# Kernel tuning notes

Measured on AMD Instinct MI355X. Metric: run time of the kernel, lower is better.

The kernel has to match this reference:

```python
import jax, jax.numpy as jnp
import numpy as np


def _ln(x):
    m = jnp.mean(x, axis=-1, keepdims=True)
    v = jnp.var(x, axis=-1, keepdims=True)
    return (x - m) * jax.lax.rsqrt(v + 1e-5)


def _forward(ql, cl, plm, ada_g_w, ada_g_b, ada_b_w, wq, bq, wk, wv, z_ln_g, z_ln_b, wz, wg, wo, sg_w, sg_b, ada2_g_w, ada2_g_b, ada2_b_w, ff1, ff2, ff3, sg2_w, sg2_b, n_queries, n_keys):
    B, N, C = ql.shape
    NB, _, D = wq.shape
    H = wz.shape[-1]
    DH = D // H
    # AF3-style 32x128 blocked local attention bias (additive mask), as in source
    centers = jnp.arange(N // n_queries + 1, dtype=jnp.float32) * n_queries + (n_queries / 2 - 0.5)
    pos = jnp.arange(N, dtype=jnp.float32)
    row = jnp.abs(pos[:, None] - centers[None, :]) < n_queries / 2   # [N, n_centers]
    col = jnp.abs(pos[:, None] - centers[None, :]) < n_keys / 2     # [N, n_centers]
    BIG = jnp.float32(1e10)
    blm = jnp.sum((row[:, None, :] & col[None, :, :]).astype(jnp.float32), axis=-1) * BIG - BIG  # [N, N], 0 or -1e10
    s_ln = _ln(cl)  # conditioning signal, shared LN across blocks
    a = ql
    for i in range(NB):  # DiffusionTransformer (AF3 Alg 23)
        # AttentionPairBias with AdaLN conditioning (Alg 24/26)
        x = jax.nn.sigmoid(s_ln @ ada_g_w[i] + ada_g_b[i]) * _ln(a) + s_ln @ ada_b_w[i]
        q = (x @ wq[i] + bq[i]).reshape(B, N, H, DH)
        k = (x @ wk[i]).reshape(B, N, H, DH)
        v = (x @ wv[i]).reshape(B, N, H, DH)
        zb = jnp.einsum('bqkc,ch->bhqk', _ln(plm) * z_ln_g[i] + z_ln_b[i], wz[i])  # pair bias
        logits = jnp.einsum('bqhd,bkhd->bhqk', q, k) * (1.0 / np.sqrt(DH)) + zb + blm[None, None]
        p = jax.nn.softmax(logits, axis=-1)
        o = jnp.einsum('bhqk,bkhd->bqhd', p, v)
        g = jax.nn.sigmoid(x @ wg[i]).reshape(B, N, H, DH)
        attn = (g * o).reshape(B, N, D) @ wo[i]
        b_out = jax.nn.sigmoid(s_ln @ sg_w[i] + sg_b[i]) * attn  # adaLN-zero style output gate
        # ConditionedTransitionBlock (Alg 25, SwiGLU)
        y = jax.nn.sigmoid(s_ln @ ada2_g_w[i] + ada2_g_b[i]) * _ln(a) + s_ln @ ada2_b_w[i]
        ff = jax.nn.silu(y @ ff1[i]) * (y @ ff2[i])
        t = jax.nn.sigmoid(s_ln @ sg2_w[i] + sg2_b[i]) * (ff @ ff3[i])
        a = b_out + t
    return a


def setup_inputs() -> dict:
    key = jax.random.key(0)
    B, N, C, CZ = 1, 3072, 128, 16
    H, DH, NB, CT = 4, 32, 3, 256  # CT = n_transition * C
    D = H * DH
    ks = jax.random.split(key, 32)
    it = iter(range(32))
    def r(shape, s=0.02):
        return jax.random.normal(ks[next(it)], shape, dtype=jnp.float32) * s
    inp = {
        'ql': jax.random.normal(ks[next(it)], (B, N, C), jnp.float32),
        'cl': jax.random.normal(ks[next(it)], (B, N, C), jnp.float32),
        'plm': jax.random.normal(ks[next(it)], (B, N, N, CZ), jnp.float32),
        'ada_g_w': r((NB, C, C)), 'ada_g_b': jnp.zeros((NB, C), jnp.float32), 'ada_b_w': r((NB, C, C)),
        'wq': r((NB, C, D)), 'bq': jnp.zeros((NB, D), jnp.float32), 'wk': r((NB, C, D)), 'wv': r((NB, C, D)),
        'z_ln_g': jnp.ones((NB, CZ), jnp.float32), 'z_ln_b': jnp.zeros((NB, CZ), jnp.float32), 'wz': r((NB, CZ, H)),
        'wg': r((NB, C, D)), 'wo': r((NB, D, C)),
        'sg_w': r((NB, C, C)), 'sg_b': jnp.full((NB, C), -2.0, jnp.float32),
        'ada2_g_w': r((NB, C, C)), 'ada2_g_b': jnp.zeros((NB, C), jnp.float32), 'ada2_b_w': r((NB, C, C)),
        'ff1': r((NB, C, CT)), 'ff2': r((NB, C, CT)), 'ff3': r((NB, CT, C)),
        'sg2_w': r((NB, C, C)), 'sg2_b': jnp.full((NB, C), -2.0, jnp.float32),
        'n_queries': 32, 'n_keys': 128,
    }
    return inp


def reference(ql, cl, plm, ada_g_w, ada_g_b, ada_b_w, wq, bq, wk, wv, z_ln_g, z_ln_b, wz, wg, wo, sg_w, sg_b, ada2_g_w, ada2_g_b, ada2_b_w, ff1, ff2, ff3, sg2_w, sg2_b, n_queries, n_keys):
    return _forward(ql, cl, plm, ada_g_w, ada_g_b, ada_b_w, wq, bq, wk, wv, z_ln_g, z_ln_b, wz, wg, wo, sg_w, sg_b, ada2_g_w, ada2_g_b, ada2_b_w, ff1, ff2, ff3, sg2_w, sg2_b, n_queries, n_keys)
```

## Files before the change

### kernel.cpp

```cpp
#include <hip/hip_runtime.h>
#include <cmath>

#define NTOK 3072
#define NBLK 3
#define PSS 133

__device__ __forceinline__ float sig(float v) { return 1.0f / (1.0f + expf(-v)); }

struct Params {
    const float *ql, *cl, *plm;
    const float *ada_g_w, *ada_g_b, *ada_b_w;
    const float *wq, *bq, *wk, *wv;
    const float *z_ln_g, *z_ln_b, *wz;
    const float *wg, *wo, *sg_w, *sg_b;
    const float *ada2_g_w, *ada2_g_b, *ada2_b_w;
    const float *ff1, *ff2, *ff3, *sg2_w, *sg2_b;
    float *qkvg, *ffb, *zb, *G, *bout4, *tpart;
    float *out;
};

__device__ __forceinline__ float4 ln_row32(float4 v)
{
    float s = v.x + v.y + v.z + v.w;
#pragma unroll
    for (int m = 1; m < 32; m <<= 1) s += __shfl_xor(s, m);
    float mean = s * (1.0f / 128.0f);
    float d0 = v.x - mean, d1 = v.y - mean, d2 = v.z - mean, d3 = v.w - mean;
    float var = d0 * d0 + d1 * d1 + d2 * d2 + d3 * d3;
#pragma unroll
    for (int m = 1; m < 32; m <<= 1) var += __shfl_xor(var, m);
    float rs = 1.0f / sqrtf(var * (1.0f / 128.0f) + 1e-5f);
    return make_float4(d0 * rs, d1 * rs, d2 * rs, d3 * rs);
}

__global__ __launch_bounds__(256) void k0_cond(Params P)
{
    int tid = threadIdx.x, bid = blockIdx.x;
    const size_t NC = (size_t)NTOK * 128;
    if (bid < 1728) {
        __shared__ __align__(16) float smA[32 * 132];
        int x8 = bid & 7, rest = bid >> 3;
        int tl = rest % 12, unit = rest / 12;
        int kind = unit % 6, i = unit / 6;
        int row0 = (x8 * 12 + tl) * 32;
#pragma unroll
        for (int it = 0; it < 4; it++) {
            int fo = (tid + it * 256) * 4, r = fo >> 7, c = fo & 127;
            *(float4*)&smA[r * 132 + c] = *(const float4*)&P.cl[(size_t)(row0 + r) * 128 + c];
        }
        __syncthreads();
        int hw = tid >> 5, cq = (tid & 31) * 4;
#pragma unroll
        for (int rr = 0; rr < 4; rr++) {
            int r = hw * 4 + rr;
            float4 n = ln_row32(*(float4*)&smA[r * 132 + cq]);
            *(float4*)&smA[r * 132 + cq] = n;
        }
        __syncthreads();
        const float* W; const float* bias = nullptr; bool dosig = false;
        switch (kind) {
            case 0:  W = P.ada_g_w  + (size_t)i * 16384; bias = P.ada_g_b  + i * 128; dosig = true; break;
            case 1:  W = P.ada_b_w  + (size_t)i * 16384; break;
            case 2:  W = P.ada2_g_w + (size_t)i * 16384; bias = P.ada2_g_b + i * 128; dosig = true; break;
            case 3:  W = P.ada2_b_w + (size_t)i * 16384; break;
            case 4:  W = P.sg_w     + (size_t)i * 16384; bias = P.sg_b     + i * 128; dosig = true; break;
            default: W = P.sg2_w    + (size_t)i * 16384; bias = P.sg2_b    + i * 128; dosig = true; break;
        }
        W += cq;
        float acc[4][4] = {};
#pragma unroll 8
        for (int k = 0; k < 128; k++) {
            float4 w4 = *(const float4*)(W + (size_t)k * 128);
#pragma unroll
            for (int rr = 0; rr < 4; rr++) {
                float a = smA[(hw * 4 + rr) * 132 + k];
                acc[rr][0] = fmaf(a, w4.x, acc[rr][0]);
                acc[rr][1] = fmaf(a, w4.y, acc[rr][1]);
                acc[rr][2] = fmaf(a, w4.z, acc[rr][2]);
                acc[rr][3] = fmaf(a, w4.w, acc[rr][3]);
            }
        }
        float4 b4 = bias ? *(const float4*)&bias[cq] : make_float4(0, 0, 0, 0);
        float* dst = P.G + (size_t)(kind * NBLK + i) * NC;
#pragma unroll
        for (int rr = 0; rr < 4; rr++) {
            float4 o = make_float4(acc[rr][0] + b4.x, acc[rr][1] + b4.y,
                                   acc[rr][2] + b4.z, acc[rr][3] + b4.w);
            if (dosig) { o.x = sig(o.x); o.y = sig(o.y); o.z = sig(o.z); o.w = sig(o.w); }
            *(float4*)&dst[(size_t)(row0 + hw * 4 + rr) * 128 + cq] = o;
        }
    } else {
        __shared__ __align__(16) float wzg[204];
        int b2 = bid - 1728;
        int x8 = b2 & 7, rest = b2 >> 3;
        int jl = rest >> 2, kkc = rest & 3;
        int j = x8 * 12 + jl;
        if (tid < 192) {
            int i3 = tid >> 6, rem = tid & 63, c = rem >> 2, h = rem & 3;
            wzg[(i3 * 16 + c) * 4 + h] = P.z_ln_g[i3 * 16 + c] * P.wz[(i3 * 16 + c) * 4 + h];
        }
        if (tid < 12) {
            int i3 = tid >> 2, h = tid & 3;
            float s = 0.0f;
            for (int c = 0; c < 16; c++) s += P.z_ln_b[i3 * 16 + c] * P.wz[(i3 * 16 + c) * 4 + h];
            wzg[192 + tid] = s;
        }
        __syncthreads();
        int kstart = max(0, j * 32 - 48);
        int W = min(NTOK, j * 32 + 80) - kstart;
#pragma unroll
        for (int it = 0; it < 4; it++) {
            int idx = tid + it * 256;
            int qi = idx >> 5, kk = kkc * 32 + (idx & 31);
            if (kk >= W) continue;
            int q = j * 32 + qi;
            const float* src = P.plm + ((size_t)q * NTOK + (size_t)(kstart + kk)) * 16;
            float xv[16];
            *(float4*)(xv + 0)  = *(const float4*)(src + 0);
            *(float4*)(xv + 4)  = *(const float4*)(src + 4);
            *(float4*)(xv + 8)  = *(const float4*)(src + 8);
            *(float4*)(xv + 12) = *(const float4*)(src + 12);
            float s = 0.0f;
#pragma unroll
            for (int c = 0; c < 16; c++) s += xv[c];
            float mean = s * (1.0f / 16.0f);
            float var = 0.0f;
#pragma unroll
            for (int c = 0; c < 16; c++) { float d = xv[c] - mean; var += d * d; }
            float rs = 1.0f / sqrtf(var * (1.0f / 16.0f) + 1e-5f);
#pragma unroll
            for (int c = 0; c < 16; c++) xv[c] = (xv[c] - mean) * rs;
#pragma unroll
            for (int i3 = 0; i3 < NBLK; i3++) {
#pragma unroll
                for (int h = 0; h < 4; h++) {
                    float o = wzg[192 + i3 * 4 + h];
#pragma unroll
                    for (int c = 0; c < 16; c++) o = fmaf(xv[c], wzg[(i3 * 16 + c) * 4 + h], o);
                    P.zb[((size_t)(i3 * 4 + h) * NTOK + q) * 128 + kk] = o;
                }
            }
        }
    }
}

__global__ __launch_bounds__(256) void kA_pre(Params P, int i)
{
    __shared__ __align__(16) float smX[32 * 132];
    const size_t NC = (size_t)NTOK * 128;
    int tid = threadIdx.x, bid = blockIdx.x;
    int x8 = bid & 7, rest = bid >> 3;
    int tl = rest % 12, u = rest / 12;
    int row0 = (x8 * 12 + tl) * 32;
    int hw = tid >> 5, cq = (tid & 31) * 4;
    const float* Gg = P.G + (size_t)(((u < 4 ? 0 : 2) * NBLK) + i) * NC;
    const float* Gb = P.G + (size_t)(((u < 4 ? 1 : 3) * NBLK) + i) * NC;
    const float* G4p = P.G + (size_t)(4 * NBLK + (i - 1)) * NC;
#pragma unroll
    for (int rr = 0; rr < 4; rr++) {
        int r = row0 + hw * 4 + rr;
        float4 a4;
        if (i == 0) {
            a4 = *(const float4*)&P.ql[(size_t)r * 128 + cq];
        } else {
            size_t off = (size_t)r * 128 + cq;
            float4 p0 = *(const float4*)&P.bout4[off];
            float4 p1 = *(const float4*)&P.bout4[NC + off];
            float4 p2 = *(const float4*)&P.bout4[2 * NC + off];
            float4 p3 = *(const float4*)&P.bout4[3 * NC + off];
            float4 tp = *(const float4*)&P.tpart[off];
            float4 gs = *(const float4*)&G4p[off];
            a4.x = fmaf(gs.x, p0.x + p1.x + p2.x + p3.x, tp.x);
            a4.y = fmaf(gs.y, p0.y + p1.y + p2.y + p3.y, tp.y);
            a4.z = fmaf(gs.z, p0.z + p1.z + p2.z + p3.z, tp.z);
            a4.w = fmaf(gs.w, p0.w + p1.w + p2.w + p3.w, tp.w);
        }
        float4 ln4 = ln_row32(a4);
        float4 g4 = *(const float4*)&Gg[(size_t)r * 128 + cq];
        float4 b4 = *(const float4*)&Gb[(size_t)r * 128 + cq];
        float4 x4;
        x4.x = fmaf(g4.x, ln4.x, b4.x);
        x4.y = fmaf(g4.y, ln4.y, b4.y);
        x4.z = fmaf(g4.z, ln4.z, b4.z);
        x4.w = fmaf(g4.w, ln4.w, b4.w);
        *(float4*)&smX[(hw * 4 + rr) * 132 + cq] = x4;
    }
    __syncthreads();
    if (u < 4) {
        const float* W = (u == 0 ? P.wq : u == 1 ? P.wk : u == 2 ? P.wv : P.wg)
                         + (size_t)i * 16384 + cq;
        float acc[4][4] = {};
#pragma unroll 8
        for (int k = 0; k < 128; k++) {
            float4 w4 = *(const float4*)(W + (size_t)k * 128);
#pragma unroll
            for (int rr = 0; rr < 4; rr++) {
                float a = smX[(hw * 4 + rr) * 132 + k];
                acc[rr][0] = fmaf(a, w4.x, acc[rr][0]);
                acc[rr][1] = fmaf(a, w4.y, acc[rr][1]);
                acc[rr][2] = fmaf(a, w4.z, acc[rr][2]);
                acc[rr][3] = fmaf(a, w4.w, acc[rr][3]);
            }
        }
        float4 b4 = (u == 0) ? *(const float4*)&P.bq[(size_t)i * 128 + cq]
                             : make_float4(0, 0, 0, 0);
#pragma unroll
        for (int rr = 0; rr < 4; rr++) {
            int r = row0 + hw * 4 + rr;
            *(float4*)&P.qkvg[(size_t)r * 512 + u * 128 + cq] =
                make_float4(acc[rr][0] + b4.x, acc[rr][1] + b4.y,
                            acc[rr][2] + b4.z, acc[rr][3] + b4.w);
        }
    } else {
        int ch = (u - 4) * 128;
        const float* W1 = P.ff1 + (size_t)i * 32768 + ch + cq;
        const float* W2 = P.ff2 + (size_t)i * 32768 + ch + cq;
        float a1[4][4] = {}, a2[4][4] = {};
#pragma unroll 4
        for (int k = 0; k < 128; k++) {
            float4 w14 = *(const float4*)(W1 + (size_t)k * 256);
            float4 w24 = *(const float4*)(W2 + (size_t)k * 256);
#pragma unroll
            for (int rr = 0; rr < 4; rr++) {
                float a = smX[(hw * 4 + rr) * 132 + k];
                a1[rr][0] = fmaf(a, w14.x, a1[rr][0]);
                a1[rr][1] = fmaf(a, w14.y, a1[rr][1]);
                a1[rr][2] = fmaf(a, w14.z, a1[rr][2]);
                a1[rr][3] = fmaf(a, w14.w, a1[rr][3]);
                a2[rr][0] = fmaf(a, w24.x, a2[rr][0]);
                a2[rr][1] = fmaf(a, w24.y, a2[rr][1]);
                a2[rr][2] = fmaf(a, w24.z, a2[rr][2]);
                a2[rr][3] = fmaf(a, w24.w, a2[rr][3]);
            }
        }
#pragma unroll
        for (int rr = 0; rr < 4; rr++) {
            int r = row0 + hw * 4 + rr;
            float4 o;
            o.x = a1[rr][0] * sig(a1[rr][0]) * a2[rr][0];
            o.y = a1[rr][1] * sig(a1[rr][1]) * a2[rr][1];
            o.z = a1[rr][2] * sig(a1[rr][2]) * a2[rr][2];
            o.w = a1[rr][3] * sig(a1[rr][3]) * a2[rr][3];
            *(float4*)&P.ffb[(size_t)r * 256 + ch + cq] = o;
        }
    }
}

__global__ __launch_bounds__(256) void kB_attn(Params P, int i)
{
    __shared__ __align__(16) float sm[11344];
    const size_t NC = (size_t)NTOK * 128;
    int tid = threadIdx.x, bid = blockIdx.x;
    if (bid < 768) {
        float* ks = sm;
        float* vs = sm + 4608;
        float* ps = sm + 9216;
        int x8 = bid & 7, g = bid >> 3;
        int jl = g >> 3, rem = g & 7;
        int h = rem >> 1, qh = rem & 1;
        int jglob = x8 * 12 + jl;
        int q0 = jglob * 32 + qh * 16;
        int kstart = max(0, jglob * 32 - 48);
        int W = min(NTOK, jglob * 32 + 80) - kstart;
        for (int idx = tid; idx < W * 8; idx += 256) {
            int kk = idx >> 3, d = (idx & 7) * 4;
            const float* base = &P.qkvg[(size_t)(kstart + kk) * 512 + 128 + h * 32 + d];
            float4 tK = *(const float4*)base;
            float4 tV = *(const float4*)(base + 128);
            *(float4*)&ks[kk * 36 + d] = tK;
            *(float4*)&vs[kk * 36 + d] = tV;
        }
        const float* zbase = &P.zb[((size_t)(i * 4 + h) * NTOK + q0) * 128];
#pragma unroll
        for (int it = 0; it < 2; it++) {
            int idx = tid + it * 256;
            int r = idx >> 5, c4 = (idx & 31) * 4;
            float4 z4 = *(const float4*)&zbase[(size_t)r * 128 + c4];
            ps[r * PSS + c4]     = z4.x;
            ps[r * PSS + c4 + 1] = z4.y;
            ps[r * PSS + c4 + 2] = z4.z;
            ps[r * PSS + c4 + 3] = z4.w;
        }
        int qi = tid & 15, kg = tid >> 4;
        float qreg[32];
        {
            const float* qp = &P.qkvg[(size_t)(q0 + qi) * 512 + h * 32];
#pragma unroll
            for (int d4 = 0; d4 < 8; d4++) {
                float4 tq = *(const float4*)(qp + d4 * 4);
                qreg[d4 * 4] = tq.x; qreg[d4 * 4 + 1] = tq.y;
                qreg[d4 * 4 + 2] = tq.z; qreg[d4 * 4 + 3] = tq.w;
            }
        }
        __syncthreads();
        const float scale = 0.17677669529663687f;
#pragma unroll
        for (int t2 = 0; t2 < 8; t2++) {
            int kk = kg + t2 * 16;
            if (kk < W) {
                float acc = 0.0f;
#pragma unroll
                for (int d4 = 0; d4 < 8; d4++) {
                    float4 kv = *(const float4*)&ks[kk * 36 + d4 * 4];
                    acc = fmaf(qreg[d4 * 4 + 0], kv.x, acc);
                    acc = fmaf(qreg[d4 * 4 + 1], kv.y, acc);
                    acc = fmaf(qreg[d4 * 4 + 2], kv.z, acc);
                    acc = fmaf(qreg[d4 * 4 + 3], kv.w, acc);
                }
                ps[qi * PSS + kk] = fmaf(acc, scale, ps[qi * PSS + kk]);
            }
        }
        __syncthreads();
        {
            int row = tid >> 4, sub = tid & 15;
            float m = -3.0e38f;
            for (int kk = sub; kk < W; kk += 16) m = fmaxf(m, ps[row * PSS + kk]);
#pragma unroll
            for (int s2 = 1; s2 < 16; s2 <<= 1) m = fmaxf(m, __shfl_xor(m, s2));
            float ssum = 0.0f;
            for (int kk = sub; kk < W; kk += 16) {
                float e = expf(ps[row * PSS + kk] - m);
                ps[row * PSS + kk] = e; ssum += e;
            }
#pragma unroll
            for (int s2 = 1; s2 < 16; s2 <<= 1) ssum += __shfl_xor(ssum, s2);
            float rinv = 1.0f / ssum;
            for (int kk = sub; kk < W; kk += 16) ps[row * PSS + kk] *= rinv;
        }
        __syncthreads();
        {
            int dg = tid >> 4, d0 = dg * 2;
            float o0 = 0.0f, o1 = 0.0f, o0b = 0.0f, o1b = 0.0f;
            for (int kk = 0; kk + 1 < W; kk += 2) {
                float p0 = ps[qi * PSS + kk], p1 = ps[qi * PSS + kk + 1];
                float2 va = *(const float2*)&vs[kk * 36 + d0];
                float2 vb = *(const float2*)&vs[(kk + 1) * 36 + d0];
                o0  = fmaf(p0, va.x, o0);  o1  = fmaf(p0, va.y, o1);
                o0b = fmaf(p1, vb.x, o0b); o1b = fmaf(p1, vb.y, o1b);
            }
            if (W & 1) {
                float p0 = ps[qi * PSS + W - 1];
                float2 va = *(const float2*)&vs[(W - 1) * 36 + d0];
                o0 = fmaf(p0, va.x, o0); o1 = fmaf(p0, va.y, o1);
            }
            o0 += o0b; o1 += o1b;
            float2 g2 = *(const float2*)&P.qkvg[(size_t)(q0 + qi) * 512 + 384 + h * 32 + d0];
            ks[qi * 33 + d0]     = o0 * sig(g2.x);
            ks[qi * 33 + d0 + 1] = o1 * sig(g2.y);
        }
        __syncthreads();
        {
            int r = tid >> 4, ci = tid & 15;
            int c0 = ci * 8;
            const float* o_s = ks;
            const float* wop = P.wo + (size_t)i * 16384 + (size_t)(h * 32) * 128 + c0;
            float acc[8] = {};
#pragma unroll 4
            for (int d = 0; d < 32; d++) {
                float a = o_s[r * 33 + d];
                float4 w0 = *(const float4*)(wop + (size_t)d * 128);
                float4 w1 = *(const float4*)(wop + (size_t)d * 128 + 4);
                acc[0] = fmaf(a, w0.x, acc[0]); acc[1] = fmaf(a, w0.y, acc[1]);
                acc[2] = fmaf(a, w0.z, acc[2]); acc[3] = fmaf(a, w0.w, acc[3]);
                acc[4] = fmaf(a, w1.x, acc[4]); acc[5] = fmaf(a, w1.y, acc[5]);
                acc[6] = fmaf(a, w1.z, acc[6]); acc[7] = fmaf(a, w1.w, acc[7]);
            }
            float* dst = P.bout4 + (size_t)h * NC + (size_t)(q0 + r) * 128 + c0;
            *(float4*)dst       = make_float4(acc[0], acc[1], acc[2], acc[3]);
            *(float4*)(dst + 4) = make_float4(acc[4], acc[5], acc[6], acc[7]);
        }
    } else {
        float* smC = sm;
        int b2 = bid - 768;
        int x8 = b2 & 7, rest = b2 >> 3;
        int tl = rest >> 1, chalf = rest & 1;
        int row0 = x8 * 384 + tl * 16;
#pragma unroll
        for (int it = 0; it < 4; it++) {
            int fo = (tid + it * 256) * 4, r = fo >> 8, c = fo & 255;
            *(float4*)&smC[r * 260 + c] = *(const float4*)&P.ffb[(size_t)(row0 + r) * 256 + c];
        }
        __syncthreads();
        int r = tid >> 4, c = chalf * 64 + (tid & 15) * 4;
        const float* f3_p = P.ff3 + (size_t)i * 32768 + c;
        float acc[4] = {};
#pragma unroll 8
        for (int k = 0; k < 256; k++) {
            float4 w4 = *(const float4*)(f3_p + (size_t)k * 128);
            float a = smC[r * 260 + k];
            acc[0] = fmaf(a, w4.x, acc[0]);
            acc[1] = fmaf(a, w4.y, acc[1]);
            acc[2] = fmaf(a, w4.z, acc[2]);
            acc[3] = fmaf(a, w4.w, acc[3]);
        }
        int row = row0 + r;
        float4 g5 = *(const float4*)&P.G[(size_t)(5 * NBLK + i) * NC + (size_t)row * 128 + c];
        *(float4*)&P.tpart[(size_t)row * 128 + c] =
            make_float4(g5.x * acc[0], g5.y * acc[1], g5.z * acc[2], g5.w * acc[3]);
    }
}

__global__ __launch_bounds__(256) void kC_out(Params P)
{
    const size_t NC = (size_t)NTOK * 128;
    int idx = blockIdx.x * 256 + threadIdx.x;
    int r = idx >> 5, cq = (idx & 31) * 4;
    size_t off = (size_t)r * 128 + cq;
    float4 p0 = *(const float4*)&P.bout4[off];
    float4 p1 = *(const float4*)&P.bout4[NC + off];
    float4 p2 = *(const float4*)&P.bout4[2 * NC + off];
    float4 p3 = *(const float4*)&P.bout4[3 * NC + off];
    float4 tp = *(const float4*)&P.tpart[off];
    float4 gs = *(const float4*)&P.G[(size_t)(4 * NBLK + (NBLK - 1)) * NC + off];
    float4 o;
    o.x = fmaf(gs.x, p0.x + p1.x + p2.x + p3.x, tp.x);
    o.y = fmaf(gs.y, p0.y + p1.y + p2.y + p3.y, tp.y);
    o.z = fmaf(gs.z, p0.z + p1.z + p2.z + p3.z, tp.z);
    o.w = fmaf(gs.w, p0.w + p1.w + p2.w + p3.w, tp.w);
    *(float4*)&P.out[off] = o;
}

extern "C" void kernel_launch(void* const* d_in, const int* in_sizes, int n_in,
                              void* d_out, int out_size, void* d_ws, size_t ws_size,
                              hipStream_t stream)
{
    Params P;
    P.ql       = (const float*)d_in[0];
    P.cl       = (const float*)d_in[1];
    P.plm      = (const float*)d_in[2];
    P.ada_g_w  = (const float*)d_in[3];
    P.ada_g_b  = (const float*)d_in[4];
    P.ada_b_w  = (const float*)d_in[5];
    P.wq       = (const float*)d_in[6];
    P.bq       = (const float*)d_in[7];
    P.wk       = (const float*)d_in[8];
    P.wv       = (const float*)d_in[9];
    P.z_ln_g   = (const float*)d_in[10];
    P.z_ln_b   = (const float*)d_in[11];
    P.wz       = (const float*)d_in[12];
    P.wg       = (const float*)d_in[13];
    P.wo       = (const float*)d_in[14];
    P.sg_w     = (const float*)d_in[15];
    P.sg_b     = (const float*)d_in[16];
    P.ada2_g_w = (const float*)d_in[17];
    P.ada2_g_b = (const float*)d_in[18];
    P.ada2_b_w = (const float*)d_in[19];
    P.ff1      = (const float*)d_in[20];
    P.ff2      = (const float*)d_in[21];
    P.ff3      = (const float*)d_in[22];
    P.sg2_w    = (const float*)d_in[23];
    P.sg2_b    = (const float*)d_in[24];

    float* ws = (float*)d_ws;
    const size_t NC = (size_t)NTOK * 128;
    P.qkvg  = ws;
    P.ffb   = ws + 4 * NC;
    P.zb    = ws + 6 * NC;
    P.G     = ws + 18 * NC;
    P.bout4 = ws + 36 * NC;
    P.tpart = ws + 40 * NC;
    P.out   = (float*)d_out;

    k0_cond<<<2112, 256, 0, stream>>>(P);
    for (int i = 0; i < NBLK; i++) {
        kA_pre<<<576, 256, 0, stream>>>(P, i);
        kB_attn<<<1152, 256, 0, stream>>>(P, i);
    }
    kC_out<<<384, 256, 0, stream>>>(P);
}
```

Baseline: 264.1 us.

## Fold deferred conditioning and pair-bias work into first pre-attention launch

The standalone conditioning kernel is reduced to computing only the block-0 AdaLN gate and shift projections. The other conditioning projections and the pair-bias computation move into the first kA_pre launch as extra thread blocks, so they run alongside block-0's QKV and FFN work. The u index is reversed so the FFN units are scheduled first. This shortens the serial prologue and fills the GPU better, at the cost of a larger, heterogeneous first launch with more shared memory per block.

```diff
diff --git a/kernel.cpp b/kernel.cpp
--- a/kernel.cpp
+++ b/kernel.cpp
@@ -33,66 +33,182 @@
     return make_float4(d0 * rs, d1 * rs, d2 * rs, d3 * rs);
 }
 
-__global__ __launch_bounds__(256) void k0_cond(Params P)
-{
+__device__ __forceinline__ void cond_unit(const Params& P, float* smA, int tid,
+                                          int kind, int i, int row0)
+{
+    const size_t NC = (size_t)NTOK * 128;
+#pragma unroll
+    for (int it = 0; it < 4; it++) {
+        int fo = (tid + it * 256) * 4, r = fo >> 7, c = fo & 127;
+        *(float4*)&smA[r * 132 + c] = *(const float4*)&P.cl[(size_t)(row0 + r) * 128 + c];
+    }
+    __syncthreads();
+    int hw = tid >> 5, cq = (tid & 31) * 4;
+#pragma unroll
+    for (int rr = 0; rr < 4; rr++) {
+        int r = hw * 4 + rr;
+        float4 n = ln_row32(*(float4*)&smA[r * 132 + cq]);
+        *(float4*)&smA[r * 132 + cq] = n;
+    }
+    __syncthreads();
+    const float* W; const float* bias = nullptr; bool dosig = false;
+    switch (kind) {
+        case 0:  W = P.ada_g_w  + (size_t)i * 16384; bias = P.ada_g_b  + i * 128; dosig = true; break;
+        case 1:  W = P.ada_b_w  + (size_t)i * 16384; break;
+        case 2:  W = P.ada2_g_w + (size_t)i * 16384; bias = P.ada2_g_b + i * 128; dosig = true; break;
+        case 3:  W = P.ada2_b_w + (size_t)i * 16384; break;
+        case 4:  W = P.sg_w     + (size_t)i * 16384; bias = P.sg_b     + i * 128; dosig = true; break;
+        default: W = P.sg2_w    + (size_t)i * 16384; bias = P.sg2_b    + i * 128; dosig = true; break;
+    }
+    W += cq;
+    float acc[4][4] = {};
+#pragma unroll 8
+    for (int k = 0; k < 128; k++) {
+        float4 w4 = *(const float4*)(W + (size_t)k * 128);
+#pragma unroll
+        for (int rr = 0; rr < 4; rr++) {
+            float a = smA[(hw * 4 + rr) * 132 + k];
+            acc[rr][0] = fmaf(a, w4.x, acc[rr][0]);
+            acc[rr][1] = fmaf(a, w4.y, acc[rr][1]);
+            acc[rr][2] = fmaf(a, w4.z, acc[rr][2]);
+            acc[rr][3] = fmaf(a, w4.w, acc[rr][3]);
+        }
+    }
+    float4 b4 = bias ? *(const float4*)&bias[cq] : make_float4(0, 0, 0, 0);
+    float* dst = P.G + (size_t)(kind * NBLK + i) * NC;
+#pragma unroll
+    for (int rr = 0; rr < 4; rr++) {
+        float4 o = make_float4(acc[rr][0] + b4.x, acc[rr][1] + b4.y,
+                               acc[rr][2] + b4.z, acc[rr][3] + b4.w);
+        if (dosig) { o.x = sig(o.x); o.y = sig(o.y); o.z = sig(o.z); o.w = sig(o.w); }
+        *(float4*)&dst[(size_t)(row0 + hw * 4 + rr) * 128 + cq] = o;
+    }
+}
+
+__global__ __launch_bounds__(256) void kInit(Params P)
+{
+    __shared__ __align__(16) float smA[32 * 132];
     int tid = threadIdx.x, bid = blockIdx.x;
+    int x8 = bid & 7, rest = bid >> 3;
+    int tl = rest % 12, kind = rest / 12;
+    int row0 = (x8 * 12 + tl) * 32;
+    cond_unit(P, smA, tid, kind, 0, row0);
+}
+
+__global__ __launch_bounds__(256) void kA_pre(Params P, int i)
+{
+    __shared__ __align__(16) float smX[32 * 132];
+    __shared__ __align__(16) float wzg[204];
     const size_t NC = (size_t)NTOK * 128;
-    if (bid < 1728) {
-        __shared__ __align__(16) float smA[32 * 132];
+    int tid = threadIdx.x, bid = blockIdx.x;
+    if (bid < 576) {
         int x8 = bid & 7, rest = bid >> 3;
+        int tl = rest % 12, u = 5 - rest / 12;
+        int row0 = (x8 * 12 + tl) * 32;
+        int hw = tid >> 5, cq = (tid & 31) * 4;
+        const float* Gg = P.G + (size_t)(((u < 4 ? 0 : 2) * NBLK) + i) * NC;
+        const float* Gb = P.G + (size_t)(((u < 4 ? 1 : 3) * NBLK) + i) * NC;
+        const float* G4p = P.G + (size_t)(4 * NBLK + (i > 0 ? i - 1 : 0)) * NC;
+#pragma unroll
+        for (int rr = 0; rr < 4; rr++) {
+            int r = row0 + hw * 4 + rr;
+            size_t off = (size_t)r * 128 + cq;
+            float4 a4;
+            if (i == 0) {
+                a4 = *(const float4*)&P.ql[off];
+            } else {
+                float4 p0 = *(const float4*)&P.bout4[off];
+                float4 p1 = *(const float4*)&P.bout4[NC + off];
+                float4 p2 = *(const float4*)&P.bout4[2 * NC + off];
+                float4 p3 = *(const float4*)&P.bout4[3 * NC + off];
+                float4 tp = *(const float4*)&P.tpart[off];
+                float4 gs = *(const float4*)&G4p[off];
+                a4.x = fmaf(gs.x, p0.x + p1.x + p2.x + p3.x, tp.x);
+                a4.y = fmaf(gs.y, p0.y + p1.y + p2.y + p3.y, tp.y);
+                a4.z = fmaf(gs.z, p0.z + p1.z + p2.z + p3.z, tp.z);
+                a4.w = fmaf(gs.w, p0.w + p1.w + p2.w + p3.w, tp.w);
+            }
+            float4 ln4 = ln_row32(a4);
+            float4 g4 = *(const float4*)&Gg[off];
+            float4 b4 = *(const float4*)&Gb[off];
+            float4 x4;
+            x4.x = fmaf(g4.x, ln4.x, b4.x);
+            x4.y = fmaf(g4.y, ln4.y, b4.y);
+            x4.z = fmaf(g4.z, ln4.z, b4.z);
+            x4.w = fmaf(g4.w, ln4.w, b4.w);
+            *(float4*)&smX[(hw * 4 + rr) * 132 + cq] = x4;
+        }
+        __syncthreads();
+        if (u < 4) {
+            const float* W = (u == 0 ? P.wq : u == 1 ? P.wk : u == 2 ? P.wv : P.wg)
+                             + (size_t)i * 16384 + cq;
+            float acc[4][4] = {};
+#pragma unroll 8
+            for (int k = 0; k < 128; k++) {
+                float4 w4 = *(const float4*)(W + (size_t)k * 128);
+#pragma unroll
+                for (int rr = 0; rr < 4; rr++) {
+                    float a = smX[(hw * 4 + rr) * 132 + k];
+                    acc[rr][0] = fmaf(a, w4.x, acc[rr][0]);
+                    acc[rr][1] = fmaf(a, w4.y, acc[rr][1]);
+                    acc[rr][2] = fmaf(a, w4.z, acc[rr][2]);
+                    acc[rr][3] = fmaf(a, w4.w, acc[rr][3]);
+                }
+            }
+            float4 b4 = (u == 0) ? *(const float4*)&P.bq[(size_t)i * 128 + cq]
+                                 : make_float4(0, 0, 0, 0);
+#pragma unroll
+            for (int rr = 0; rr < 4; rr++) {
+                int r = row0 + hw * 4 + rr;
+                *(float4*)&P.qkvg[(size_t)r * 512 + u * 128 + cq] =
+                    make_float4(acc[rr][0] + b4.x, acc[rr][1] + b4.y,
+                                acc[rr][2] + b4.z, acc[rr][3] + b4.w);
+            }
+        } else {
+            int ch = (u - 4) * 128;
+            const float* W1 = P.ff1 + (size_t)i * 32768 + ch + cq;
+            const float* W2 = P.ff2 + (size_t)i * 32768 + ch + cq;
+            float a1[4][4] = {}, a2[4][4] = {};
+#pragma unroll 4
+            for (int k = 0; k < 128; k++) {
+                float4 w14 = *(const float4*)(W1 + (size_t)k * 256);
+                float4 w24 = *(const float4*)(W2 + (size_t)k * 256);
+#pragma unroll
+                for (int rr = 0; rr < 4; rr++) {
+                    float a = smX[(hw * 4 + rr) * 132 + k];
+                    a1[rr][0] = fmaf(a, w14.x, a1[rr][0]);
+                    a1[rr][1] = fmaf(a, w14.y, a1[rr][1]);
+                    a1[rr][2] = fmaf(a, w14.z, a1[rr][2]);
+                    a1[rr][3] = fmaf(a, w14.w, a1[rr][3]);
+                    a2[rr][0] = fmaf(a, w24.x, a2[rr][0]);
+                    a2[rr][1] = fmaf(a, w24.y, a2[rr][1]);
+                    a2[rr][2] = fmaf(a, w24.z, a2[rr][2]);
+                    a2[rr][3] = fmaf(a, w24.w, a2[rr][3]);
+                }
+            }
+#pragma unroll
+            for (int rr = 0; rr < 4; rr++) {
+                int r = row0 + hw * 4 + rr;
+                float4 o;
+                o.x = a1[rr][0] * sig(a1[rr][0]) * a2[rr][0];
+                o.y = a1[rr][1] * sig(a1[rr][1]) * a2[rr][1];
+                o.z = a1[rr][2] * sig(a1[rr][2]) * a2[rr][2];
+                o.w = a1[rr][3] * sig(a1[rr][3]) * a2[rr][3];
+                *(float4*)&P.ffb[(size_t)r * 256 + ch + cq] = o;
+            }
+        }
+    } else if (bid < 1920) {
+        int b2 = bid - 576;
+        int x8 = b2 & 7, rest = b2 >> 3;
         int tl = rest % 12, unit = rest / 12;
-        int kind = unit % 6, i = unit / 6;
+        int kind, il;
+        if (unit < 8) { kind = unit >> 1; il = 1 + (unit & 1); }
+        else          { int v = unit - 8; kind = 4 + v / 3; il = v % 3; }
         int row0 = (x8 * 12 + tl) * 32;
-#pragma unroll
-        for (int it = 0; it < 4; it++) {
-            int fo = (tid + it * 256) * 4, r = fo >> 7, c = fo & 127;
-            *(float4*)&smA[r * 132 + c] = *(const float4*)&P.cl[(size_t)(row0 + r) * 128 + c];
-        }
-        __syncthreads();
-        int hw = tid >> 5, cq = (tid & 31) * 4;
-#pragma unroll
-        for (int rr = 0; rr < 4; rr++) {
-            int r = hw * 4 + rr;
-            float4 n = ln_row32(*(float4*)&smA[r * 132 + cq]);
-            *(float4*)&smA[r * 132 + cq] = n;
-        }
-        __syncthreads();
-        const float* W; const float* bias = nullptr; bool dosig = false;
-        switch (kind) {
-            case 0:  W = P.ada_g_w  + (size_t)i * 16384; bias = P.ada_g_b  + i * 128; dosig = true; break;
-            case 1:  W = P.ada_b_w  + (size_t)i * 16384; break;
-            case 2:  W = P.ada2_g_w + (size_t)i * 16384; bias = P.ada2_g_b + i * 128; dosig = true; break;
-            case 3:  W = P.ada2_b_w + (size_t)i * 16384; break;
-            case 4:  W = P.sg_w     + (size_t)i * 16384; bias = P.sg_b     + i * 128; dosig = true; break;
-            default: W = P.sg2_w    + (size_t)i * 16384; bias = P.sg2_b    + i * 128; dosig = true; break;
-        }
-        W += cq;
-        float acc[4][4] = {};
-#pragma unroll 8
-        for (int k = 0; k < 128; k++) {
-            float4 w4 = *(const float4*)(W + (size_t)k * 128);
-#pragma unroll
-            for (int rr = 0; rr < 4; rr++) {
-                float a = smA[(hw * 4 + rr) * 132 + k];
-                acc[rr][0] = fmaf(a, w4.x, acc[rr][0]);
-                acc[rr][1] = fmaf(a, w4.y, acc[rr][1]);
-                acc[rr][2] = fmaf(a, w4.z, acc[rr][2]);
-                acc[rr][3] = fmaf(a, w4.w, acc[rr][3]);
-            }
-        }
-        float4 b4 = bias ? *(const float4*)&bias[cq] : make_float4(0, 0, 0, 0);
-        float* dst = P.G + (size_t)(kind * NBLK + i) * NC;
-#pragma unroll
-        for (int rr = 0; rr < 4; rr++) {
-            float4 o = make_float4(acc[rr][0] + b4.x, acc[rr][1] + b4.y,
-                                   acc[rr][2] + b4.z, acc[rr][3] + b4.w);
-            if (dosig) { o.x = sig(o.x); o.y = sig(o.y); o.z = sig(o.z); o.w = sig(o.w); }
-            *(float4*)&dst[(size_t)(row0 + hw * 4 + rr) * 128 + cq] = o;
-        }
+        cond_unit(P, smX, tid, kind, il, row0);
     } else {
-        __shared__ __align__(16) float wzg[204];
-        int b2 = bid - 1728;
-        int x8 = b2 & 7, rest = b2 >> 3;
+        int b3 = bid - 1920;
+        int x8 = b3 & 7, rest = b3 >> 3;
         int jl = rest >> 2, kkc = rest & 3;
         int j = x8 * 12 + jl;
         if (tid < 192) {
@@ -140,108 +256,6 @@
                     P.zb[((size_t)(i3 * 4 + h) * NTOK + q) * 128 + kk] = o;
                 }
             }
-        }
-    }
-}
-
-__global__ __launch_bounds__(256) void kA_pre(Params P, int i)
-{
-    __shared__ __align__(16) float smX[32 * 132];
-    const size_t NC = (size_t)NTOK * 128;
-    int tid = threadIdx.x, bid = blockIdx.x;
-    int x8 = bid & 7, rest = bid >> 3;
-    int tl = rest % 12, u = rest / 12;
-    int row0 = (x8 * 12 + tl) * 32;
-    int hw = tid >> 5, cq = (tid & 31) * 4;
-    const float* Gg = P.G + (size_t)(((u < 4 ? 0 : 2) * NBLK) + i) * NC;
-    const float* Gb = P.G + (size_t)(((u < 4 ? 1 : 3) * NBLK) + i) * NC;
-    const float* G4p = P.G + (size_t)(4 * NBLK + (i - 1)) * NC;
-#pragma unroll
-    for (int rr = 0; rr < 4; rr++) {
-        int r = row0 + hw * 4 + rr;
-        float4 a4;
-        if (i == 0) {
-            a4 = *(const float4*)&P.ql[(size_t)r * 128 + cq];
-        } else {
-            size_t off = (size_t)r * 128 + cq;
-            float4 p0 = *(const float4*)&P.bout4[off];
-            float4 p1 = *(const float4*)&P.bout4[NC + off];
-            float4 p2 = *(const float4*)&P.bout4[2 * NC + off];
-            float4 p3 = *(const float4*)&P.bout4[3 * NC + off];
-            float4 tp = *(const float4*)&P.tpart[off];
-            float4 gs = *(const float4*)&G4p[off];
-            a4.x = fmaf(gs.x, p0.x + p1.x + p2.x + p3.x, tp.x);
-            a4.y = fmaf(gs.y, p0.y + p1.y + p2.y + p3.y, tp.y);
-            a4.z = fmaf(gs.z, p0.z + p1.z + p2.z + p3.z, tp.z);
-            a4.w = fmaf(gs.w, p0.w + p1.w + p2.w + p3.w, tp.w);
-        }
-        float4 ln4 = ln_row32(a4);
-        float4 g4 = *(const float4*)&Gg[(size_t)r * 128 + cq];
-        float4 b4 = *(const float4*)&Gb[(size_t)r * 128 + cq];
-        float4 x4;
-        x4.x = fmaf(g4.x, ln4.x, b4.x);
-        x4.y = fmaf(g4.y, ln4.y, b4.y);
-        x4.z = fmaf(g4.z, ln4.z, b4.z);
-        x4.w = fmaf(g4.w, ln4.w, b4.w);
-        *(float4*)&smX[(hw * 4 + rr) * 132 + cq] = x4;
-    }
-    __syncthreads();
-    if (u < 4) {
-        const float* W = (u == 0 ? P.wq : u == 1 ? P.wk : u == 2 ? P.wv : P.wg)
-                         + (size_t)i * 16384 + cq;
-        float acc[4][4] = {};
-#pragma unroll 8
-        for (int k = 0; k < 128; k++) {
-            float4 w4 = *(const float4*)(W + (size_t)k * 128);
-#pragma unroll
-            for (int rr = 0; rr < 4; rr++) {
-                float a = smX[(hw * 4 + rr) * 132 + k];
-                acc[rr][0] = fmaf(a, w4.x, acc[rr][0]);
-                acc[rr][1] = fmaf(a, w4.y, acc[rr][1]);
-                acc[rr][2] = fmaf(a, w4.z, acc[rr][2]);
-                acc[rr][3] = fmaf(a, w4.w, acc[rr][3]);
-            }
-        }
-        float4 b4 = (u == 0) ? *(const float4*)&P.bq[(size_t)i * 128 + cq]
-                             : make_float4(0, 0, 0, 0);
-#pragma unroll
-        for (int rr = 0; rr < 4; rr++) {
-            int r = row0 + hw * 4 + rr;
-            *(float4*)&P.qkvg[(size_t)r * 512 + u * 128 + cq] =
-                make_float4(acc[rr][0] + b4.x, acc[rr][1] + b4.y,
-                            acc[rr][2] + b4.z, acc[rr][3] + b4.w);
-        }
-    } else {
-        int ch = (u - 4) * 128;
-        const float* W1 = P.ff1 + (size_t)i * 32768 + ch + cq;
-        const float* W2 = P.ff2 + (size_t)i * 32768 + ch + cq;
-        float a1[4][4] = {}, a2[4][4] = {};
-#pragma unroll 4
-        for (int k = 0; k < 128; k++) {
-            float4 w14 = *(const float4*)(W1 + (size_t)k * 256);
-            float4 w24 = *(const float4*)(W2 + (size_t)k * 256);
-#pragma unroll
-            for (int rr = 0; rr < 4; rr++) {
-                float a = smX[(hw * 4 + rr) * 132 + k];
-                a1[rr][0] = fmaf(a, w14.x, a1[rr][0]);
-                a1[rr][1] = fmaf(a, w14.y, a1[rr][1]);
-                a1[rr][2] = fmaf(a, w14.z, a1[rr][2]);
-                a1[rr][3] = fmaf(a, w14.w, a1[rr][3]);
-                a2[rr][0] = fmaf(a, w24.x, a2[rr][0]);
-                a2[rr][1] = fmaf(a, w24.y, a2[rr][1]);
-                a2[rr][2] = fmaf(a, w24.z, a2[rr][2]);
-                a2[rr][3] = fmaf(a, w24.w, a2[rr][3]);
-            }
-        }
-#pragma unroll
-        for (int rr = 0; rr < 4; rr++) {
-            int r = row0 + hw * 4 + rr;
-            float4 o;
-            o.x = a1[rr][0] * sig(a1[rr][0]) * a2[rr][0];
-            o.y = a1[rr][1] * sig(a1[rr][1]) * a2[rr][1];
-            o.z = a1[rr][2] * sig(a1[rr][2]) * a2[rr][2];
-            o.w = a1[rr][3] * sig(a1[rr][3]) * a2[rr][3];
-            *(float4*)&P.ffb[(size_t)r * 256 + ch + cq] = o;
         }
     }
 }
@@ -461,9 +475,9 @@
     P.tpart = ws + 40 * NC;
     P.out   = (float*)d_out;
 
-    k0_cond<<<2112, 256, 0, stream>>>(P);
+    kInit<<<384, 256, 0, stream>>>(P);
     for (int i = 0; i < NBLK; i++) {
-        kA_pre<<<576, 256, 0, stream>>>(P, i);
+        kA_pre<<<(i == 0 ? 2304 : 576), 256, 0, stream>>>(P, i);
         kB_attn<<<1152, 256, 0, stream>>>(P, i);
     }
     kC_out<<<384, 256, 0, stream>>>(P);
```

Result: slower. 276.4 us (+4.6%).
